# Kernel optimization log

Hardware: AMD Instinct MI355X
Metric: run time of the kernel (lower is better)

Reference implementation:

```python
import jax, jax.numpy as jnp
import numpy as np

N = 10000        # nodes
E = 320000       # edges (avg degree 32)
NF_IN = 256
NF_OUT = 512
EPS = 1e-5


def batch_norm(x, gamma, beta):
    # BatchNorm1d training-mode: biased stats over the node (batch) dim
    mu = jnp.mean(x, axis=0)
    var = jnp.var(x, axis=0)
    return (x - mu) * jax.lax.rsqrt(var + EPS) * gamma + beta


def sage_conv(x, src, dst, W_l, W_r, bias):
    # PyG SAGEConv, aggr='mean': out = lin_l(mean_{j->i} x_j) + lin_r(x_i)
    msg = x[src]                                             # [E, F]
    s = jax.ops.segment_sum(msg, dst, num_segments=N)        # [N, F]
    cnt = jax.ops.segment_sum(jnp.ones((msg.shape[0], 1), x.dtype), dst, num_segments=N)
    mean = s / jnp.maximum(cnt, 1.0)
    return mean @ W_l + bias + x @ W_r


def setup_inputs() -> dict:
    key = jax.random.key(0)
    ks = jax.random.split(key, 8)
    x = jax.random.normal(ks[0], (N, NF_IN), jnp.float32)
    edge_index = jax.random.randint(ks[1], (2, E), 0, N, dtype=jnp.int64)
    s_in = 0.02
    return {
        "x": x,
        "edge_index": edge_index,
        "gamma0": jnp.ones((NF_IN,), jnp.float32),
        "beta0": jnp.zeros((NF_IN,), jnp.float32),
        "W0_l": jax.random.normal(ks[2], (NF_IN, NF_OUT), jnp.float32) * s_in,
        "W0_r": jax.random.normal(ks[3], (NF_IN, NF_OUT), jnp.float32) * s_in,
        "bias0": jnp.zeros((NF_OUT,), jnp.float32),
        "gamma1": jnp.ones((NF_OUT,), jnp.float32),
        "beta1": jnp.zeros((NF_OUT,), jnp.float32),
        "W1_l": jax.random.normal(ks[4], (NF_OUT, NF_OUT), jnp.float32) * s_in,
        "W1_r": jax.random.normal(ks[5], (NF_OUT, NF_OUT), jnp.float32) * s_in,
        "bias1": jnp.zeros((NF_OUT,), jnp.float32),
        "W_sc": jax.random.normal(ks[6], (NF_IN, NF_OUT), jnp.float32) * s_in,
        "b_sc": jnp.zeros((NF_OUT,), jnp.float32),
    }


def reference(x, edge_index, gamma0, beta0, W0_l, W0_r, bias0,
              gamma1, beta1, W1_l, W1_r, bias1, W_sc, b_sc):
    src, dst = edge_index[0], edge_index[1]
    h = jax.nn.relu(batch_norm(x, gamma0, beta0))
    h = sage_conv(h, src, dst, W0_l, W0_r, bias0)
    h = jax.nn.relu(batch_norm(h, gamma1, beta1))
    h = sage_conv(h, src, dst, W1_l, W1_r, bias1)
    x_sc = x @ W_sc + b_sc  # nin_shortcut since nf_in != nf_out
    return x_sc + h
```

## Files before the change

### kernel.cpp

```cpp
#include <hip/hip_runtime.h>
#include <hip/hip_bf16.h>
#include <cstdint>
#include <cstddef>

#define N_NODES 10000
#define N_EDGES 320000
#define FIN 256
#define FOUT 512
#define BN_EPS 1e-5f
#define DEG_CAP 96
#define SLICE_CAP 18
#define NRANGES 20
#define NSLICES 16
#define NODES_PER_RANGE (N_NODES / NRANGES)
#define EDGES_PER_SLICE (N_EDGES / NSLICES)
#define SCAN_BLOCKS (NRANGES * NSLICES)

typedef unsigned short ushort_t;
typedef unsigned char uchar_t;
typedef __attribute__((ext_vector_type(8))) short short8;
typedef __attribute__((ext_vector_type(4))) float f32x4;
typedef __attribute__((ext_vector_type(2))) float f32x2;
typedef __attribute__((ext_vector_type(4))) unsigned short ushort4v;
typedef __attribute__((ext_vector_type(8))) unsigned short ushort8v;

__device__ inline ushort_t f2bf(float f) {
  __hip_bfloat16 h = __float2bfloat16(f);
  return *reinterpret_cast<ushort_t*>(&h);
}
__device__ inline float bf2f(ushort_t u) {
  union { unsigned int i; float f; } c;
  c.i = ((unsigned int)u) << 16;
  return c.f;
}
__device__ inline uchar_t f2q(float v) {
  return (uchar_t)(__builtin_amdgcn_cvt_pk_fp8_f32(v, v, 0u, false) & 0xffu);
}
__device__ inline void q4_to_f32(unsigned int w, float* o) {
  f32x2 lo = __builtin_amdgcn_cvt_pk_f32_fp8(w, false);
  f32x2 hi = __builtin_amdgcn_cvt_pk_f32_fp8(w, true);
  o[0] = lo[0]; o[1] = lo[1]; o[2] = hi[0]; o[3] = hi[1];
}

__global__ void zero_k(int* __restrict__ p, int n) {
  int i = blockIdx.x * blockDim.x + threadIdx.x;
  if (i < n) p[i] = 0;
}

__global__ __launch_bounds__(256)
void prologue_k(const int* __restrict__ src, const int* __restrict__ dst,
                int* __restrict__ fill, int* __restrict__ csrc,
                const float* __restrict__ W0l, const float* __restrict__ W0r,
                const float* __restrict__ Wsc, const float* __restrict__ W1l,
                const float* __restrict__ W1r, const float* __restrict__ bias1,
                const float* __restrict__ bsc,
                ushort_t* __restrict__ w0lt, ushort_t* __restrict__ w0rt,
                ushort_t* __restrict__ wsct, ushort_t* __restrict__ w1lt,
                ushort_t* __restrict__ w1rt, float* __restrict__ cbias,
                const float* __restrict__ x, float* __restrict__ sums0,
                ushort_t* __restrict__ xb, uchar_t* __restrict__ xq) {
  __shared__ __align__(16) char smem[512 * 4 + NODES_PER_RANGE * SLICE_CAP * 4];
  int b = blockIdx.x;
  int tid = threadIdx.x;

  if (b < SCAN_BLOCKS) {
    int range = b / NSLICES;
    int slice = b % NSLICES;
    int lo = range * NODES_PER_RANGE;
    int* lcnt = (int*)smem;
    int* lbuf = lcnt + 512;
    for (int i = tid; i < NODES_PER_RANGE; i += 256) lcnt[i] = 0;
    __syncthreads();

    int e0 = slice * EDGES_PER_SLICE;
    const int4* dst4 = (const int4*)(dst + e0);
    const int4* src4 = (const int4*)(src + e0);
    const int nvec = EDGES_PER_SLICE / 4;
    for (int v = tid; v < nvec; v += 256) {
      int4 d4 = dst4[v];
      int4 s4 = src4[v];
      int dd[4] = {d4.x, d4.y, d4.z, d4.w};
      int ss[4] = {s4.x, s4.y, s4.z, s4.w};
#pragma unroll
      for (int j = 0; j < 4; ++j) {
        int d = dd[j] - lo;
        if (d >= 0 && d < NODES_PER_RANGE) {
          int pos = atomicAdd(&lcnt[d], 1);
          if (pos < SLICE_CAP) lbuf[d * SLICE_CAP + pos] = ss[j];
        }
      }
    }
    __syncthreads();

    for (int i = tid; i < NODES_PER_RANGE; i += 256) {
      int cnt = min(lcnt[i], SLICE_CAP);
      if (cnt > 0) {
        int off = atomicAdd(&fill[lo + i], cnt);
        int wmax = min(cnt, DEG_CAP - off);
        for (int k = 0; k < wmax; ++k)
          csrc[(size_t)(lo + i) * DEG_CAP + off + k] = lbuf[i * SLICE_CAP + k];
      }
    }
    return;
  }

  if (b < SCAN_BLOCKS + 897) {
    int bb = b - SCAN_BLOCKS;
    if (bb == 896) {
      cbias[tid] = bias1[tid] + bsc[tid];
      cbias[tid + 256] = bias1[tid + 256] + bsc[tid + 256];
      return;
    }
    const float* W;
    ushort_t* Wt;
    int K, t;
    if (bb < 384) {
      K = 256; t = bb & 127;
      if (bb < 128)      { W = W0l; Wt = w0lt; }
      else if (bb < 256) { W = W0r; Wt = w0rt; }
      else               { W = Wsc; Wt = wsct; }
    } else {
      K = 512; t = (bb - 384) & 255;
      if (bb < 640) { W = W1l; Wt = w1lt; }
      else          { W = W1r; Wt = w1rt; }
    }
    ushort_t (*tl)[40] = (ushort_t(*)[40])smem;
    int Kt = K >> 5;
    int bk = (t % Kt) * 32, bn = (t / Kt) * 32;
    int tx = tid & 31, ty = tid >> 5;
#pragma unroll
    for (int i = 0; i < 4; ++i)
      tl[ty + i * 8][tx] = f2bf(W[(size_t)(bk + ty + i * 8) * 512 + bn + tx]);
    __syncthreads();
#pragma unroll
    for (int i = 0; i < 4; ++i)
      Wt[(size_t)(bn + ty + i * 8) * K + bk + tx] = tl[tx][ty + i * 8];
    return;
  }

  int blk = b - (SCAN_BLOCKS + 897);
  int c = tid;
  int r0 = blk * 80, r1 = r0 + 80;
  float s = 0.f, q = 0.f;
  for (int r = r0; r < r1; ++r) {
    float v = x[(size_t)r * FIN + c];
    s += v;
    q = fmaf(v, v, q);
    xb[(size_t)r * FIN + c] = f2bf(v);
    xq[(size_t)r * FIN + c] = f2q(v);
  }
  atomicAdd(&sums0[c], s);
  atomicAdd(&sums0[FIN + c], q);
}

template <int F>
__global__ __launch_bounds__(64)
void gather_mean_q8(const uchar_t* __restrict__ H, const int* __restrict__ fill,
                    const int* __restrict__ csrc, const float* __restrict__ sums,
                    const float* __restrict__ gamma, const float* __restrict__ beta,
                    float invN, ushort_t* __restrict__ agg) {
  constexpr int VEC = F / 64;
  int node = blockIdx.x;
  int c0 = threadIdx.x * VEC;
  float sc[VEC], sh[VEC];
#pragma unroll
  for (int j = 0; j < VEC; ++j) {
    float mu = sums[c0 + j] * invN;
    float var = fmaf(-mu, mu, sums[F + c0 + j] * invN);
    float s = rsqrtf(var + BN_EPS) * gamma[c0 + j];
    sc[j] = s;
    sh[j] = fmaf(-mu, s, beta[c0 + j]);
  }
  int deg = fill[node];
  int lim = min(deg, DEG_CAP);
  const int* cs = csrc + (size_t)node * DEG_CAP;
  float acc[VEC] = {};
  int e = 0;
  for (; e + 2 <= lim; e += 2) {
    int s0 = cs[e], s1 = cs[e + 1];
    float va[VEC], vb[VEC];
    if constexpr (VEC == 8) {
      uint2 ua = *(const uint2*)&H[(size_t)s0 * F + c0];
      uint2 ub = *(const uint2*)&H[(size_t)s1 * F + c0];
      q4_to_f32(ua.x, va); q4_to_f32(ua.y, va + 4);
      q4_to_f32(ub.x, vb); q4_to_f32(ub.y, vb + 4);
    } else {
      unsigned int ua = *(const unsigned int*)&H[(size_t)s0 * F + c0];
      unsigned int ub = *(const unsigned int*)&H[(size_t)s1 * F + c0];
      q4_to_f32(ua, va);
      q4_to_f32(ub, vb);
    }
#pragma unroll
    for (int j = 0; j < VEC; ++j)
      acc[j] += fmaxf(fmaf(va[j], sc[j], sh[j]), 0.f) +
                fmaxf(fmaf(vb[j], sc[j], sh[j]), 0.f);
  }
  if (e < lim) {
    int s0 = cs[e];
    float va[VEC];
    if constexpr (VEC == 8) {
      uint2 ua = *(const uint2*)&H[(size_t)s0 * F + c0];
      q4_to_f32(ua.x, va); q4_to_f32(ua.y, va + 4);
    } else {
      unsigned int ua = *(const unsigned int*)&H[(size_t)s0 * F + c0];
      q4_to_f32(ua, va);
    }
#pragma unroll
    for (int j = 0; j < VEC; ++j) acc[j] += fmaxf(fmaf(va[j], sc[j], sh[j]), 0.f);
  }
  float ic = 1.0f / fmaxf((float)deg, 1.0f);
  if constexpr (VEC == 8) {
    ushort8v o;
#pragma unroll
    for (int j = 0; j < 8; ++j) o[j] = f2bf(acc[j] * ic);
    *(ushort8v*)&agg[(size_t)node * F + c0] = o;
  } else {
    ushort4v o;
#pragma unroll
    for (int j = 0; j < 4; ++j) o[j] = f2bf(acc[j] * ic);
    *(ushort4v*)&agg[(size_t)node * F + c0] = o;
  }
}

template <int EPI, int K0, int K1, int K2, bool STATS, int BNS, int KBN, bool WQ>
__global__ __launch_bounds__(512)
void gemm_mfma(const ushort_t* __restrict__ A0, const ushort_t* __restrict__ B0,
               const ushort_t* __restrict__ A1p, const ushort_t* __restrict__ B1p,
               const ushort_t* __restrict__ A2p, const ushort_t* __restrict__ B2p,
               const float* __restrict__ bias, void* __restrict__ Cv,
               uchar_t* __restrict__ Cq, int M,
               const float* __restrict__ sums, const float* __restrict__ gamma,
               const float* __restrict__ beta, float invN,
               float* __restrict__ statsOut) {
  __shared__ __align__(16) short As[64][72];
  __shared__ __align__(16) short Bs[128][72];
  __shared__ float ab_s[2 * KBN];

  int wgid = blockIdx.x;
  int cxcd = wgid & 7;
  int j = wgid >> 3;
  int nt = j & 3;
  int yhi = j >> 2;
  int y = cxcd + yhi * 8;
  int MT = (M + 63) >> 6;
  if (y >= MT) return;
  int m0 = y * 64;
  int n0 = nt * 128;

  int tid = threadIdx.x;
  int lane = tid & 63;
  int w = tid >> 6;
  int wm = w >> 2, wn = w & 3;

  if constexpr (BNS >= 0) {
    for (int c = tid; c < KBN; c += 512) {
      float mu = sums[c] * invN;
      float var = fmaf(-mu, mu, sums[KBN + c] * invN);
      float s = rsqrtf(var + BN_EPS) * gamma[c];
      ab_s[c] = s;
      ab_s[KBN + c] = fmaf(-mu, s, beta[c]);
    }
    __syncthreads();
  }

  int ar = tid >> 3;
  int aq8 = (tid & 7) * 8;
  int br = tid >> 2;
  int bq = (tid & 3) * 16;
  bool arow_ok = (m0 + ar) < M;

  constexpr int NS = (K0 + K1 + K2) / 64;
  f32x4 acc[2][2] = {};

  short8 ra0, rb0, rb1;
  bool dobn_cur = false;
  int aboff_cur = 0;

  auto LOADSTEP = [&](int ks) {
    int k0 = ks * 64;
    const ushort_t* Ap;
    const ushort_t* Bp;
    int lk, KA;
    if (k0 < K0) { Ap = A0; Bp = B0; lk = k0; KA = K0; dobn_cur = (BNS == 0); }
    else if (k0 < K0 + K1) { Ap = A1p; Bp = B1p; lk = k0 - K0; KA = K1; dobn_cur = (BNS == 1); }
    else { Ap = A2p; Bp = B2p; lk = k0 - K0 - K1; KA = K2; dobn_cur = (BNS == 2); }
    aboff_cur = lk;
    if (arow_ok) {
      ra0 = *(const short8*)&Ap[(size_t)(m0 + ar) * KA + lk + aq8];
    } else {
      ra0 = short8{};
    }
    const short8* bp = (const short8*)&Bp[(size_t)(n0 + br) * KA + lk + bq];
    rb0 = bp[0]; rb1 = bp[1];
  };

  LOADSTEP(0);
  for (int ks = 0; ks < NS; ++ks) {
    if constexpr (BNS >= 0) {
      if (dobn_cur && arow_ok) {
        const float* abp = &ab_s[aboff_cur + aq8];
#pragma unroll
        for (int jj = 0; jj < 8; ++jj)
          ra0[jj] = (short)f2bf(fmaxf(fmaf(bf2f((ushort_t)ra0[jj]), abp[jj], abp[KBN + jj]), 0.f));
      }
    }
    *(short8*)&As[ar][aq8] = ra0;
    *(short8*)&Bs[br][bq] = rb0;
    *(short8*)&Bs[br][bq + 8] = rb1;
    __syncthreads();

    if (ks + 1 < NS) LOADSTEP(ks + 1);

#pragma unroll
    for (int ks2 = 0; ks2 < 2; ++ks2) {
      int kof = ks2 * 32 + (lane >> 4) * 8;
      int rsel = lane & 15;
      short8 af[2], bfv[2];
      af[0] = *(const short8*)&As[wm * 32 + rsel][kof];
      af[1] = *(const short8*)&As[wm * 32 + 16 + rsel][kof];
      bfv[0] = *(const short8*)&Bs[wn * 32 + rsel][kof];
      bfv[1] = *(const short8*)&Bs[wn * 32 + 16 + rsel][kof];
#pragma unroll
      for (int mi = 0; mi < 2; ++mi)
#pragma unroll
        for (int ni = 0; ni < 2; ++ni)
          acc[mi][ni] = __builtin_amdgcn_mfma_f32_16x16x32_bf16(
              af[mi], bfv[ni], acc[mi][ni], 0, 0, 0);
    }
    __syncthreads();
  }

  float* st = (float*)&As[0][0];
  if constexpr (STATS) {
    if (tid < 256) st[tid] = 0.f;
    __syncthreads();
  }

  int colbase = n0 + wn * 32 + (lane & 15);
  int rowq = (lane >> 4) * 4;
#pragma unroll
  for (int ni = 0; ni < 2; ++ni) {
    int col = colbase + ni * 16;
    float bv = bias[col];
    float s_l = 0.f, q_l = 0.f;
#pragma unroll
    for (int mi = 0; mi < 2; ++mi) {
      int rbase = m0 + wm * 32 + mi * 16 + rowq;
#pragma unroll
      for (int r = 0; r < 4; ++r) {
        int row = rbase + r;
        if (row < M) {
          float v = acc[mi][ni][r] + bv;
          if constexpr (STATS) {
            s_l += v;
            q_l = fmaf(v, v, q_l);
          }
          if constexpr (EPI == 0) {
            ((ushort_t*)Cv)[(size_t)row * 512 + col] = f2bf(v);
            if constexpr (WQ) Cq[(size_t)row * 512 + col] = f2q(v);
          } else {
            ((float*)Cv)[(size_t)row * 512 + col] = v;
          }
        }
      }
    }
    if constexpr (STATS) {
      int cloc = wn * 32 + ni * 16 + (lane & 15);
      atomicAdd(&st[cloc], s_l);
      atomicAdd(&st[128 + cloc], q_l);
    }
  }
  if constexpr (STATS) {
    __syncthreads();
    if (tid < 256) {
      int c = tid & 127;
      atomicAdd(&statsOut[(tid >> 7) * 512 + n0 + c], st[(tid >> 7) * 128 + c]);
    }
  }
}

extern "C" void kernel_launch(void* const* d_in, const int* in_sizes, int n_in,
                              void* d_out, int out_size, void* d_ws, size_t ws_size,
                              hipStream_t stream) {
  const float* x = (const float*)d_in[0];
  const int* ei = (const int*)d_in[1];
  const int* src = ei;
  const int* dst = ei + N_EDGES;
  const float* gamma0 = (const float*)d_in[2];
  const float* beta0  = (const float*)d_in[3];
  const float* W0l    = (const float*)d_in[4];
  const float* W0r    = (const float*)d_in[5];
  const float* bias0  = (const float*)d_in[6];
  const float* gamma1 = (const float*)d_in[7];
  const float* beta1  = (const float*)d_in[8];
  const float* W1l    = (const float*)d_in[9];
  const float* W1r    = (const float*)d_in[10];
  const float* bias1  = (const float*)d_in[11];
  const float* Wsc    = (const float*)d_in[12];
  const float* bsc    = (const float*)d_in[13];
  float* out = (float*)d_out;

  char* wp = (char*)d_ws;
  ushort_t* agg0b = (ushort_t*)wp; wp += (size_t)N_NODES * FIN * 2;
  ushort_t* h1b   = (ushort_t*)wp; wp += (size_t)N_NODES * FOUT * 2;
  ushort_t* agg1b = (ushort_t*)wp; wp += (size_t)N_NODES * FOUT * 2;
  ushort_t* xb    = (ushort_t*)wp; wp += (size_t)N_NODES * FIN * 2;
  uchar_t*  xq    = (uchar_t*)wp;  wp += (size_t)N_NODES * FIN;
  uchar_t*  h1q   = (uchar_t*)wp;  wp += (size_t)N_NODES * FOUT;
  ushort_t* w0lt  = (ushort_t*)wp; wp += (size_t)FIN * FOUT * 2;
  ushort_t* w0rt  = (ushort_t*)wp; wp += (size_t)FIN * FOUT * 2;
  ushort_t* wsct  = (ushort_t*)wp; wp += (size_t)FIN * FOUT * 2;
  ushort_t* w1lt  = (ushort_t*)wp; wp += (size_t)FOUT * FOUT * 2;
  ushort_t* w1rt  = (ushort_t*)wp; wp += (size_t)FOUT * FOUT * 2;
  float* cbias = (float*)wp; wp += FOUT * 4;
  float* sums0 = (float*)wp; wp += 2 * FIN * 4;
  float* sums1 = (float*)wp; wp += 2 * FOUT * 4;
  int* fill    = (int*)wp; wp += (size_t)N_NODES * 4;
  int* csrc    = (int*)wp; wp += (size_t)N_NODES * DEG_CAP * 4;

  const float invN = 1.0f / N_NODES;

  const int zwords = 2 * FIN + 2 * FOUT + N_NODES;
  zero_k<<<(zwords + 255) / 256, 256, 0, stream>>>((int*)sums0, zwords);

  prologue_k<<<SCAN_BLOCKS + 897 + 125, 256, 0, stream>>>(
      src, dst, fill, csrc, W0l, W0r, Wsc, W1l, W1r, bias1, bsc,
      w0lt, w0rt, wsct, w1lt, w1rt, cbias, x, sums0, xb, xq);

  gather_mean_q8<FIN><<<N_NODES, 64, 0, stream>>>(
      xq, fill, csrc, sums0, gamma0, beta0, invN, agg0b);

  const int GEMM_GRID = 8 * 4 * ((((N_NODES + 63) / 64) + 7) / 8);

  gemm_mfma<0, FIN, FIN, 0, true, 1, FIN, true>
      <<<GEMM_GRID, 512, 0, stream>>>(
      agg0b, w0lt, xb, w0rt, nullptr, nullptr, bias0, h1b, h1q, N_NODES,
      sums0, gamma0, beta0, invN, sums1);

  gather_mean_q8<FOUT><<<N_NODES, 64, 0, stream>>>(
      h1q, fill, csrc, sums1, gamma1, beta1, invN, agg1b);

  gemm_mfma<1, FOUT, FOUT, FIN, false, 1, FOUT, false>
      <<<GEMM_GRID, 512, 0, stream>>>(
      agg1b, w1lt, h1b, w1rt, xb, wsct, cbias, out, nullptr, N_NODES,
      sums1, gamma1, beta1, invN, nullptr);
}
```

Before: 126.0 us.

## Restructure GEMM to 4 waves with 32x32 MFMA, double-buffered swizzled LDS

The GEMM kernel drops from 512 to 256 threads. Each wave now computes a 32x64 tile with two 32x32x16 bf16 MFMAs instead of four 16x16x32 ones. LDS is double-buffered with an XOR swizzle replacing the padding, so the next tile is stored after the compute and only one barrier per k-step is needed. This cuts LDS reads per MFMA and sync overhead, at the cost of more registers per thread and fewer waves to hide latency.

```diff
diff --git a/kernel.cpp b/kernel.cpp
--- a/kernel.cpp
+++ b/kernel.cpp
@@ -19,7 +19,7 @@
 typedef unsigned short ushort_t;
 typedef unsigned char uchar_t;
 typedef __attribute__((ext_vector_type(8))) short short8;
-typedef __attribute__((ext_vector_type(4))) float f32x4;
+typedef __attribute__((ext_vector_type(16))) float f32x16;
 typedef __attribute__((ext_vector_type(2))) float f32x2;
 typedef __attribute__((ext_vector_type(4))) unsigned short ushort4v;
 typedef __attribute__((ext_vector_type(8))) unsigned short ushort8v;
@@ -223,7 +223,7 @@
 }
 
 template <int EPI, int K0, int K1, int K2, bool STATS, int BNS, int KBN, bool WQ>
-__global__ __launch_bounds__(512)
+__global__ __launch_bounds__(256)
 void gemm_mfma(const ushort_t* __restrict__ A0, const ushort_t* __restrict__ B0,
                const ushort_t* __restrict__ A1p, const ushort_t* __restrict__ B1p,
                const ushort_t* __restrict__ A2p, const ushort_t* __restrict__ B2p,
@@ -232,16 +232,17 @@
                const float* __restrict__ sums, const float* __restrict__ gamma,
                const float* __restrict__ beta, float invN,
                float* __restrict__ statsOut) {
-  __shared__ __align__(16) short As[64][72];
-  __shared__ __align__(16) short Bs[128][72];
+  constexpr int ABYTES = 64 * 128;
+  constexpr int BBYTES = 128 * 128;
+  __shared__ __align__(16) char Asm[2 * ABYTES];
+  __shared__ __align__(16) char Bsm[2 * BBYTES];
   __shared__ float ab_s[2 * KBN];
 
   int wgid = blockIdx.x;
   int cxcd = wgid & 7;
   int j = wgid >> 3;
   int nt = j & 3;
-  int yhi = j >> 2;
-  int y = cxcd + yhi * 8;
+  int y = cxcd + (j >> 2) * 8;
   int MT = (M + 63) >> 6;
   if (y >= MT) return;
   int m0 = y * 64;
@@ -250,10 +251,10 @@
   int tid = threadIdx.x;
   int lane = tid & 63;
   int w = tid >> 6;
-  int wm = w >> 2, wn = w & 3;
+  int wm = w >> 1, wn = w & 1;
 
   if constexpr (BNS >= 0) {
-    for (int c = tid; c < KBN; c += 512) {
+    for (int c = tid; c < KBN; c += 256) {
       float mu = sums[c] * invN;
       float var = fmaf(-mu, mu, sums[KBN + c] * invN);
       float s = rsqrtf(var + BN_EPS) * gamma[c];
@@ -263,16 +264,16 @@
     __syncthreads();
   }
 
-  int ar = tid >> 3;
-  int aq8 = (tid & 7) * 8;
-  int br = tid >> 2;
-  int bq = (tid & 3) * 16;
+  int ar = tid >> 2;
+  int aqe = (tid & 3) * 16;
+  int br = tid >> 1;
+  int bqe = (tid & 1) * 32;
   bool arow_ok = (m0 + ar) < M;
 
   constexpr int NS = (K0 + K1 + K2) / 64;
-  f32x4 acc[2][2] = {};
-
-  short8 ra0, rb0, rb1;
+  f32x16 acc0 = {}, acc1 = {};
+
+  short8 ra[2], rb[4];
   bool dobn_cur = false;
   int aboff_cur = 0;
 
@@ -286,86 +287,105 @@
     else { Ap = A2p; Bp = B2p; lk = k0 - K0 - K1; KA = K2; dobn_cur = (BNS == 2); }
     aboff_cur = lk;
     if (arow_ok) {
-      ra0 = *(const short8*)&Ap[(size_t)(m0 + ar) * KA + lk + aq8];
+      const short8* ap = (const short8*)&Ap[(size_t)(m0 + ar) * KA + lk + aqe];
+      ra[0] = ap[0]; ra[1] = ap[1];
     } else {
-      ra0 = short8{};
-    }
-    const short8* bp = (const short8*)&Bp[(size_t)(n0 + br) * KA + lk + bq];
-    rb0 = bp[0]; rb1 = bp[1];
+      ra[0] = short8{}; ra[1] = short8{};
+    }
+    const short8* bp = (const short8*)&Bp[(size_t)(n0 + br) * KA + lk + bqe];
+    rb[0] = bp[0]; rb[1] = bp[1]; rb[2] = bp[2]; rb[3] = bp[3];
   };
 
-  LOADSTEP(0);
-  for (int ks = 0; ks < NS; ++ks) {
+  int aswz = (ar & 7) << 4;
+  int bswz = (br & 7) << 4;
+
+  auto STORESTEP = [&](int buf) {
     if constexpr (BNS >= 0) {
       if (dobn_cur && arow_ok) {
-        const float* abp = &ab_s[aboff_cur + aq8];
-#pragma unroll
-        for (int jj = 0; jj < 8; ++jj)
-          ra0[jj] = (short)f2bf(fmaxf(fmaf(bf2f((ushort_t)ra0[jj]), abp[jj], abp[KBN + jj]), 0.f));
+#pragma unroll
+        for (int g = 0; g < 2; ++g) {
+          const float* abp = &ab_s[aboff_cur + aqe + g * 8];
+#pragma unroll
+          for (int jj = 0; jj < 8; ++jj)
+            ra[g][jj] = (short)f2bf(fmaxf(
+                fmaf(bf2f((ushort_t)ra[g][jj]), abp[jj], abp[KBN + jj]), 0.f));
+        }
       }
     }
-    *(short8*)&As[ar][aq8] = ra0;
-    *(short8*)&Bs[br][bq] = rb0;
-    *(short8*)&Bs[br][bq + 8] = rb1;
-    __syncthreads();
-
+    int abase = buf * ABYTES + ar * 128;
+    int bbase = buf * BBYTES + br * 128;
+#pragma unroll
+    for (int g = 0; g < 2; ++g) {
+      int cb = (aqe + g * 8) * 2;
+      *(short8*)(Asm + abase + (cb ^ aswz)) = ra[g];
+    }
+#pragma unroll
+    for (int g = 0; g < 4; ++g) {
+      int cb = (bqe + g * 8) * 2;
+      *(short8*)(Bsm + bbase + (cb ^ bswz)) = rb[g];
+    }
+  };
+
+  LOADSTEP(0);
+  STORESTEP(0);
+  __syncthreads();
+
+  int arow = wm * 32 + (lane & 31);
+  int brow0 = wn * 64 + (lane & 31);
+  int brow1 = brow0 + 32;
+  int aswzr = (arow & 7) << 4;
+  int bswzr = (brow0 & 7) << 4;
+
+  for (int ks = 0; ks < NS; ++ks) {
     if (ks + 1 < NS) LOADSTEP(ks + 1);
-
-#pragma unroll
-    for (int ks2 = 0; ks2 < 2; ++ks2) {
-      int kof = ks2 * 32 + (lane >> 4) * 8;
-      int rsel = lane & 15;
-      short8 af[2], bfv[2];
-      af[0] = *(const short8*)&As[wm * 32 + rsel][kof];
-      af[1] = *(const short8*)&As[wm * 32 + 16 + rsel][kof];
-      bfv[0] = *(const short8*)&Bs[wn * 32 + rsel][kof];
-      bfv[1] = *(const short8*)&Bs[wn * 32 + 16 + rsel][kof];
-#pragma unroll
-      for (int mi = 0; mi < 2; ++mi)
-#pragma unroll
-        for (int ni = 0; ni < 2; ++ni)
-          acc[mi][ni] = __builtin_amdgcn_mfma_f32_16x16x32_bf16(
-              af[mi], bfv[ni], acc[mi][ni], 0, 0, 0);
-    }
-    __syncthreads();
-  }
-
-  float* st = (float*)&As[0][0];
+    int abase = (ks & 1) * ABYTES + arow * 128;
+    int bbase0 = (ks & 1) * BBYTES + brow0 * 128;
+    int bbase1 = (ks & 1) * BBYTES + brow1 * 128;
+#pragma unroll
+    for (int kc = 0; kc < 4; ++kc) {
+      int kb = kc * 32 + (lane >> 5) * 16;
+      short8 af = *(const short8*)(Asm + abase + (kb ^ aswzr));
+      short8 bf0 = *(const short8*)(Bsm + bbase0 + (kb ^ bswzr));
+      short8 bf1 = *(const short8*)(Bsm + bbase1 + (kb ^ bswzr));
+      acc0 = __builtin_amdgcn_mfma_f32_32x32x16_bf16(af, bf0, acc0, 0, 0, 0);
+      acc1 = __builtin_amdgcn_mfma_f32_32x32x16_bf16(af, bf1, acc1, 0, 0, 0);
+    }
+    if (ks + 1 < NS) STORESTEP((ks + 1) & 1);
+    __syncthreads();
+  }
+
+  float* st = (float*)Asm;
   if constexpr (STATS) {
     if (tid < 256) st[tid] = 0.f;
     __syncthreads();
   }
 
-  int colbase = n0 + wn * 32 + (lane & 15);
-  int rowq = (lane >> 4) * 4;
+  int colb = n0 + wn * 64 + (lane & 31);
+  int rquad = (lane >> 5) * 4;
 #pragma unroll
   for (int ni = 0; ni < 2; ++ni) {
-    int col = colbase + ni * 16;
+    int col = colb + ni * 32;
     float bv = bias[col];
     float s_l = 0.f, q_l = 0.f;
 #pragma unroll
-    for (int mi = 0; mi < 2; ++mi) {
-      int rbase = m0 + wm * 32 + mi * 16 + rowq;
-#pragma unroll
-      for (int r = 0; r < 4; ++r) {
-        int row = rbase + r;
-        if (row < M) {
-          float v = acc[mi][ni][r] + bv;
-          if constexpr (STATS) {
-            s_l += v;
-            q_l = fmaf(v, v, q_l);
-          }
-          if constexpr (EPI == 0) {
-            ((ushort_t*)Cv)[(size_t)row * 512 + col] = f2bf(v);
-            if constexpr (WQ) Cq[(size_t)row * 512 + col] = f2q(v);
-          } else {
-            ((float*)Cv)[(size_t)row * 512 + col] = v;
-          }
+    for (int reg = 0; reg < 16; ++reg) {
+      int row = m0 + wm * 32 + (reg & 3) + 8 * (reg >> 2) + rquad;
+      if (row < M) {
+        float v = (ni == 0 ? acc0[reg] : acc1[reg]) + bv;
+        if constexpr (STATS) {
+          s_l += v;
+          q_l = fmaf(v, v, q_l);
+        }
+        if constexpr (EPI == 0) {
+          ((ushort_t*)Cv)[(size_t)row * 512 + col] = f2bf(v);
+          if constexpr (WQ) Cq[(size_t)row * 512 + col] = f2q(v);
+        } else {
+          ((float*)Cv)[(size_t)row * 512 + col] = v;
         }
       }
     }
     if constexpr (STATS) {
-      int cloc = wn * 32 + ni * 16 + (lane & 15);
+      int cloc = wn * 64 + ni * 32 + (lane & 31);
       atomicAdd(&st[cloc], s_l);
       atomicAdd(&st[128 + cloc], q_l);
     }
@@ -433,7 +453,7 @@
   const int GEMM_GRID = 8 * 4 * ((((N_NODES + 63) / 64) + 7) / 8);
 
   gemm_mfma<0, FIN, FIN, 0, true, 1, FIN, true>
-      <<<GEMM_GRID, 512, 0, stream>>>(
+      <<<GEMM_GRID, 256, 0, stream>>>(
       agg0b, w0lt, xb, w0rt, nullptr, nullptr, bias0, h1b, h1q, N_NODES,
       sums0, gamma0, beta0, invN, sums1);
 
@@ -441,7 +461,7 @@
       h1q, fill, csrc, sums1, gamma1, beta1, invN, agg1b);
 
   gemm_mfma<1, FOUT, FOUT, FIN, false, 1, FOUT, false>
-      <<<GEMM_GRID, 512, 0, stream>>>(
+      <<<GEMM_GRID, 256, 0, stream>>>(
       agg1b, w1lt, h1b, w1rt, xb, wsct, cbias, out, nullptr, N_NODES,
       sums1, gamma1, beta1, invN, nullptr);
 }
```

Result: faster. 121.9 us (-3.3%).
